# Kernel optimization log

Measured on AMD Instinct MI355X. Metric: run time of the kernel, lower is better.

## Reference

```python
import jax, jax.numpy as jnp
import numpy as np

EMBED_DIM = 1024
HEAD_DIM = 64


def setup_inputs() -> dict:
    key = jax.random.key(0)
    ks = jax.random.split(key, 7)
    s_in = EMBED_DIM ** -0.5  # torch Linear default init scale
    x = jax.random.normal(ks[0], (4, 4096, EMBED_DIM), dtype=jnp.float32)
    Wk = jax.random.uniform(ks[1], (HEAD_DIM, EMBED_DIM), jnp.float32, -s_in, s_in)
    bk = jax.random.uniform(ks[2], (HEAD_DIM,), jnp.float32, -s_in, s_in)
    Wq = jax.random.uniform(ks[3], (HEAD_DIM, EMBED_DIM), jnp.float32, -s_in, s_in)
    bq = jax.random.uniform(ks[4], (HEAD_DIM,), jnp.float32, -s_in, s_in)
    Wv = jax.random.uniform(ks[5], (HEAD_DIM, EMBED_DIM), jnp.float32, -s_in, s_in)
    bv = jax.random.uniform(ks[6], (HEAD_DIM,), jnp.float32, -s_in, s_in)
    return {"x": x, "Wq": Wq, "bq": bq, "Wk": Wk, "bk": bk, "Wv": Wv, "bv": bv}


def reference(x, Wq, bq, Wk, bk, Wv, bv):
    # torch Linear: y = x @ W.T + b
    q = jnp.einsum('btc,dc->btd', x, Wq) + bq  # [B,T,D]
    k = jnp.einsum('btc,dc->btd', x, Wk) + bk
    v = jnp.einsum('btc,dc->btd', x, Wv) + bv
    scale = HEAD_DIM ** -0.5
    # NOTE: original divides by scale (multiplies by sqrt(head_dim)) -- faithful
    scores = jnp.einsum('btd,bsd->bts', q, k) / scale  # [B,T,T]
    attn_weights = jax.nn.softmax(scores, axis=-1)
    return jnp.einsum('bts,bsd->btd', attn_weights, v)
```

## Files before the change

### kernel.cpp

```cpp
#include <hip/hip_runtime.h>

#define BATCH 4
#define SEQ   4096
#define CDIM  1024
#define DDIM  64
#define NROW  (BATCH * SEQ)
#define NSPL  8
#define SEG   (NROW * DDIM)

typedef _Float16 f16;
typedef _Float16 f16x8 __attribute__((ext_vector_type(8)));
typedef _Float16 f16x4 __attribute__((ext_vector_type(4)));
typedef __fp16   h16x2 __attribute__((ext_vector_type(2)));
typedef float    f32x4 __attribute__((ext_vector_type(4)));

#define MFMA32(a, b, c) __builtin_amdgcn_mfma_f32_16x16x32_f16((a), (b), (c), 0, 0, 0)
#define MFMA16(a, b, c) __builtin_amdgcn_mfma_f32_16x16x16f16((a), (b), (c), 0, 0, 0)

#define GLDS(g, l)                                                            \
  __builtin_amdgcn_global_load_lds((const __attribute__((address_space(1))) void*)(g), \
                                   (__attribute__((address_space(3))) void*)(l), 16, 0, 0)

#define QSCALE 11.5415603f

__device__ inline f16x8 cvt8(f32x4 a, f32x4 b) {
  h16x2 p0 = __builtin_amdgcn_cvt_pkrtz(a[0], a[1]);
  h16x2 p1 = __builtin_amdgcn_cvt_pkrtz(a[2], a[3]);
  h16x2 p2 = __builtin_amdgcn_cvt_pkrtz(b[0], b[1]);
  h16x2 p3 = __builtin_amdgcn_cvt_pkrtz(b[2], b[3]);
  f16x8 r;
  r[0] = p0[0]; r[1] = p0[1]; r[2] = p1[0]; r[3] = p1[1];
  r[4] = p2[0]; r[5] = p2[1]; r[6] = p3[0]; r[7] = p3[1];
  return r;
}

__device__ inline f16x4 cvt4(float a, float b, float c, float d) {
  h16x2 lo = __builtin_amdgcn_cvt_pkrtz(a, b);
  h16x2 hi = __builtin_amdgcn_cvt_pkrtz(c, d);
  f16x4 r;
  r[0] = lo[0]; r[1] = lo[1]; r[2] = hi[0]; r[3] = hi[1];
  return r;
}

__global__ __launch_bounds__(256) void prep_w_kernel(const float* __restrict__ Wq,
                                                     const float* __restrict__ Wk,
                                                     const float* __restrict__ Wv,
                                                     f16* __restrict__ wf2) {
  const int t = blockIdx.x * 256 + threadIdx.x;
  const int lane = t & 63;
  const int s = t >> 6;
  const int mt = s >> 5, ck = s & 31;
  const int mat = mt >> 2, tile = mt & 3;
  const int n = lane & 15, quad = lane >> 4;
  const float* W = (mat == 0) ? Wq : (mat == 1) ? Wk : Wv;
  const float* src = W + (size_t)(tile * 16 + n) * CDIM + ck * 32 + quad * 8;
  const f32x4 a = *(const f32x4*)src;
  const f32x4 b = *(const f32x4*)(src + 4);
  *(f16x8*)(wf2 + (size_t)t * 8) = cvt8(a, b);
}

__global__ __launch_bounds__(256, 4) void proj_kernel(const float* __restrict__ x,
                                                      const f16* __restrict__ wf2,
                                                      const float* __restrict__ bq,
                                                      const float* __restrict__ bk,
                                                      const float* __restrict__ bv,
                                                      f16* __restrict__ qs,
                                                      f16* __restrict__ ks,
                                                      f16* __restrict__ vc) {
  __shared__ __attribute__((aligned(16))) char lx[2][8192];
  const int tid = threadIdx.x, lane = tid & 63, w = tid >> 6;
  const int n = lane & 15, quad = lane >> 4;
  const int rowbase = blockIdx.x * 16;
  const int mtb = 3 * w;

  const float* xsrc[2];
#pragma unroll
  for (int j = 0; j < 2; ++j) {
    const int id = 2 * w + j;
    const int r = id * 2 + (lane >> 5);
    const int c = (lane & 31) ^ r;
    xsrc[j] = x + (size_t)(rowbase + r) * CDIM + c * 4;
  }

  auto issue = [&](int ck, int b) {
    char* base = &lx[b][0];
#pragma unroll
    for (int j = 0; j < 2; ++j)
      GLDS(xsrc[j] + ck * 128, base + (2 * w + j) * 1024);
  };

  const f16* wl = wf2 + (size_t)mtb * 16384 + lane * 8;

  f32x4 acc[3];
#pragma unroll
  for (int i = 0; i < 3; ++i) acc[i] = (f32x4){0.f, 0.f, 0.f, 0.f};

  issue(0, 0);
  for (int ck = 0; ck < 8; ++ck) {
    const int b = ck & 1;
    __syncthreads();
    if (ck + 1 < 8) issue(ck + 1, b ^ 1);
    const char* xb = &lx[b][0] + n * 512;
#pragma unroll
    for (int kk = 0; kk < 4; ++kk) {
      const int c1 = kk * 8 + quad * 2;
      const f32x4 xa = *(const f32x4*)(xb + ((c1 ^ n) << 4));
      const f32x4 xc = *(const f32x4*)(xb + (((c1 + 1) ^ n) << 4));
      const f16x8 af = cvt8(xa, xc);
      const f16* wq = wl + (size_t)(ck * 4 + kk) * 512;
      const f16x8 w0 = *(const f16x8*)(wq);
      const f16x8 w1 = *(const f16x8*)(wq + 16384);
      const f16x8 w2 = *(const f16x8*)(wq + 32768);
      acc[0] = MFMA32(af, w0, acc[0]);
      acc[1] = MFMA32(af, w1, acc[1]);
      acc[2] = MFMA32(af, w2, acc[2]);
    }
  }

  const int r0 = rowbase + quad * 4;
#pragma unroll
  for (int i2 = 0; i2 < 3; ++i2) {
    const int mt = mtb + i2;
    const int mat = mt >> 2, tile = mt & 3;
    const int d = tile * 16 + n;
    const f32x4 aa = acc[i2];
    if (mat == 0) {
      const float bi = bq[d];
#pragma unroll
      for (int r = 0; r < 4; ++r)
        qs[(size_t)(r0 + r) * DDIM + d] = (f16)((aa[r] + bi) * QSCALE);
    } else if (mat == 1) {
      const float bi = bk[d];
#pragma unroll
      for (int r = 0; r < 4; ++r) {
        const int tt = r0 + r;
        const int col = ((((d >> 3) ^ (tt & 7)) << 3) | (d & 7));
        ks[(size_t)tt * DDIM + col] = (f16)(aa[r] + bi);
      }
    } else {
      const float bi = bv[d];
      const int bb = r0 >> 12;
      const int tl = r0 & (SEQ - 1);
      const int ck2 = tl >> 6;
      const int bsw = (((tl & 63) >> 2) ^ n) << 2;
      *(f16x4*)(vc + ((size_t)(bb * 64 + ck2) * 64 + d) * 64 + bsw) =
          cvt4(aa[0] + bi, aa[1] + bi, aa[2] + bi, aa[3] + bi);
    }
  }
}

template <int NSPLIT>
__global__ __launch_bounds__(256, 4) void attn_kernel(const f16* __restrict__ qs,
                                                      const f16* __restrict__ ks,
                                                      const f16* __restrict__ vc,
                                                      float* __restrict__ outp,
                                                      f16* __restrict__ pacc,
                                                      float* __restrict__ pm,
                                                      float* __restrict__ pl) {
  __shared__ __attribute__((aligned(16))) f16 lk[2][4096];
  __shared__ __attribute__((aligned(16))) f16 lv[2][4096];
  const int tid = threadIdx.x, lane = tid & 63, w = tid >> 6;
  const int n = lane & 15, quad = lane >> 4;
  const int split = blockIdx.x % NSPLIT;
  const int rowblk = blockIdx.x / NSPLIT;
  const int row0 = rowblk * 128 + w * 32;
  const int bb = row0 >> 12;
  const int kbase = split * (SEQ / NSPLIT);
  const int kc0 = kbase >> 6;
  const int NC = SEQ / NSPLIT / 64;

  const f16* ksb = ks + (size_t)bb * SEQ * DDIM;
  const f16* vcb = vc + (size_t)bb * 64 * 4096;

  auto issue = [&](int c, int buf) {
#pragma unroll
    for (int i = 0; i < 2; ++i) {
      const int id = 2 * w + i;
      GLDS(ksb + (size_t)(kbase + c * 64) * 64 + id * 512 + lane * 8, &lk[buf][id * 512]);
      GLDS(vcb + (size_t)(kc0 + c) * 4096 + id * 512 + lane * 8, &lv[buf][id * 512]);
    }
  };

  f16x8 qf[2][2];
#pragma unroll
  for (int g = 0; g < 2; ++g)
#pragma unroll
    for (int hh = 0; hh < 2; ++hh)
      qf[g][hh] = *(const f16x8*)(qs + (size_t)(row0 + g * 16 + n) * DDIM + hh * 32 + quad * 8);

  const int kswz = (quad ^ (n & 7)) << 3;
  int vswz[4];
#pragma unroll
  for (int st = 0; st < 4; ++st) vswz[st] = ((((st << 2) | quad) ^ n) << 2);

  f32x4 acc[2][4];
  float m[2] = {-1e30f, -1e30f}, ll[2] = {0.f, 0.f};
#pragma unroll
  for (int g = 0; g < 2; ++g)
#pragma unroll
    for (int t = 0; t < 4; ++t) acc[g][t] = (f32x4){0.f, 0.f, 0.f, 0.f};

  issue(0, 0);
  for (int c = 0; c < NC; ++c) {
    const int b = c & 1;
    __syncthreads();
    if (c + 1 < NC) issue(c + 1, b ^ 1);

    f32x4 s[2][4];
#pragma unroll
    for (int st = 0; st < 4; ++st) {
      const f16* lkr = &lk[b][(st * 16 + n) * 64];
      const f16x8 klo = *(const f16x8*)(lkr + kswz);
      const f16x8 khi = *(const f16x8*)(lkr + (kswz ^ 32));
#pragma unroll
      for (int g = 0; g < 2; ++g) {
        f32x4 z = (f32x4){0.f, 0.f, 0.f, 0.f};
        z = MFMA32(klo, qf[g][0], z);
        s[g][st] = MFMA32(khi, qf[g][1], z);
      }
    }

    f16x4 pq[2][4];
#pragma unroll
    for (int g = 0; g < 2; ++g) {
      f32x4 mx;
#pragma unroll
      for (int r = 0; r < 4; ++r)
        mx[r] = fmaxf(fmaxf(s[g][0][r], s[g][1][r]), fmaxf(s[g][2][r], s[g][3][r]));
      float mloc = fmaxf(fmaxf(mx[0], mx[1]), fmaxf(mx[2], mx[3]));
      mloc = fmaxf(mloc, __shfl_xor(mloc, 16));
      mloc = fmaxf(mloc, __shfl_xor(mloc, 32));
      const float mnew = fmaxf(m[g], mloc);
      const float alpha = __builtin_amdgcn_exp2f(m[g] - mnew);
      m[g] = mnew;
      float psum = 0.f;
#pragma unroll
      for (int st = 0; st < 4; ++st) {
        f32x4 p;
#pragma unroll
        for (int r = 0; r < 4; ++r) p[r] = __builtin_amdgcn_exp2f(s[g][st][r] - mnew);
        psum += (p[0] + p[1]) + (p[2] + p[3]);
        pq[g][st] = cvt4(p[0], p[1], p[2], p[3]);
      }
      ll[g] = ll[g] * alpha + psum;
#pragma unroll
      for (int t = 0; t < 4; ++t) acc[g][t] *= alpha;
    }

#pragma unroll
    for (int dt = 0; dt < 4; ++dt) {
      const f16* lvr = &lv[b][(dt * 16 + n) * 64];
#pragma unroll
      for (int st = 0; st < 4; ++st) {
        const f16x4 va = *(const f16x4*)(lvr + vswz[st]);
        acc[0][dt] = MFMA16(va, pq[0][st], acc[0][dt]);
        acc[1][dt] = MFMA16(va, pq[1][st], acc[1][dt]);
      }
    }
  }

  float lred[2];
#pragma unroll
  for (int g = 0; g < 2; ++g) {
    float l = ll[g];
    l += __shfl_xor(l, 16);
    l += __shfl_xor(l, 32);
    lred[g] = l;
  }

  if (NSPLIT == 1) {
#pragma unroll
    for (int g = 0; g < 2; ++g) {
      const float inv = 1.0f / lred[g];
      const int q = row0 + g * 16 + n;
#pragma unroll
      for (int t = 0; t < 4; ++t) {
        f32x4 o = acc[g][t];
#pragma unroll
        for (int r = 0; r < 4; ++r) o[r] *= inv;
        *(f32x4*)(outp + (size_t)q * DDIM + t * 16 + quad * 4) = o;
      }
    }
  } else {
#pragma unroll
    for (int g = 0; g < 2; ++g) {
      const int q = row0 + g * 16 + n;
#pragma unroll
      for (int t = 0; t < 4; ++t)
        *(f16x4*)(pacc + ((size_t)split * NROW + q) * DDIM + t * 16 + quad * 4) =
            cvt4(acc[g][t][0], acc[g][t][1], acc[g][t][2], acc[g][t][3]);
      if (quad == 0) {
        pm[split * NROW + q] = m[g];
        pl[split * NROW + q] = lred[g];
      }
    }
  }
}

template <int NSPLIT>
__global__ __launch_bounds__(256) void combine_kernel(const f16* __restrict__ pacc,
                                                      const float* __restrict__ pm,
                                                      const float* __restrict__ pl,
                                                      float* __restrict__ out) {
  const int idx = blockIdx.x * 256 + threadIdx.x;
  const int row = idx >> 4;
  const int c = (idx & 15) * 4;
  float mm = pm[row];
#pragma unroll
  for (int s = 1; s < NSPLIT; ++s) mm = fmaxf(mm, pm[s * NROW + row]);
  float L = 0.f;
  f32x4 o = (f32x4){0.f, 0.f, 0.f, 0.f};
#pragma unroll
  for (int s = 0; s < NSPLIT; ++s) {
    const float e = __builtin_amdgcn_exp2f(pm[s * NROW + row] - mm);
    L += pl[s * NROW + row] * e;
    const f16x4 a = *(const f16x4*)(pacc + ((size_t)s * NROW + row) * DDIM + c);
#pragma unroll
    for (int j = 0; j < 4; ++j) o[j] += (float)a[j] * e;
  }
  const float inv = 1.0f / L;
#pragma unroll
  for (int j = 0; j < 4; ++j) o[j] *= inv;
  *(f32x4*)(out + (size_t)row * DDIM + c) = o;
}

extern "C" void kernel_launch(void* const* d_in, const int* in_sizes, int n_in,
                              void* d_out, int out_size, void* d_ws, size_t ws_size,
                              hipStream_t stream) {
  const float* x  = (const float*)d_in[0];
  const float* Wq = (const float*)d_in[1];
  const float* bq = (const float*)d_in[2];
  const float* Wk = (const float*)d_in[3];
  const float* bk = (const float*)d_in[4];
  const float* Wv = (const float*)d_in[5];
  const float* bv = (const float*)d_in[6];
  float* out = (float*)d_out;

  f16* wf2 = (f16*)d_ws;
  f16* qs = wf2 + 3 * 65536;
  f16* ks = qs + (size_t)SEG;
  f16* vc = ks + (size_t)SEG;
  f16* pacc = vc + (size_t)SEG;
  float* pm = (float*)(pacc + (size_t)NSPL * SEG);
  float* pl = pm + (size_t)NSPL * NROW;
  const size_t need = (size_t)((char*)(pl + (size_t)NSPL * NROW) - (char*)d_ws);

  prep_w_kernel<<<dim3(96), dim3(256), 0, stream>>>(Wq, Wk, Wv, wf2);
  proj_kernel<<<dim3(NROW / 16), dim3(256), 0, stream>>>(x, wf2, bq, bk, bv, qs, ks, vc);

  if (ws_size >= need) {
    attn_kernel<NSPL><<<dim3(128 * NSPL), dim3(256), 0, stream>>>(qs, ks, vc, nullptr, pacc, pm, pl);
    combine_kernel<NSPL><<<dim3(NROW * 16 / 256), dim3(256), 0, stream>>>(pacc, pm, pl, out);
  } else {
    attn_kernel<1><<<dim3(128), dim3(256), 0, stream>>>(qs, ks, vc, out, nullptr, nullptr, nullptr);
  }
}
```

Measured before the change: 154.5 us.

## Triple-buffer LDS prefetch with explicit vmcnt waits in projection and attention

Both the projection and attention kernels move from double to triple buffering of the LDS tiles. Loads now run two chunks ahead, and the code waits with explicit s_waitcnt vmcnt counts plus raw s_barrier instead of __syncthreads. The aim is to hide more global-to-LDS latency behind MFMA work. In exchange, the attention kernel uses more shared memory (48KB), so its launch bound drops to 3 blocks per CU, and the hand-written vmcnt counts depend on the exact number of load instructions issued.

```diff
diff --git a/kernel.cpp b/kernel.cpp
--- a/kernel.cpp
+++ b/kernel.cpp
@@ -67,7 +67,7 @@
                                                       f16* __restrict__ qs,
                                                       f16* __restrict__ ks,
                                                       f16* __restrict__ vc) {
-  __shared__ __attribute__((aligned(16))) char lx[2][8192];
+  __shared__ __attribute__((aligned(16))) char lx[3 * 8192];
   const int tid = threadIdx.x, lane = tid & 63, w = tid >> 6;
   const int n = lane & 15, quad = lane >> 4;
   const int rowbase = blockIdx.x * 16;
@@ -82,8 +82,8 @@
     xsrc[j] = x + (size_t)(rowbase + r) * CDIM + c * 4;
   }
 
-  auto issue = [&](int ck, int b) {
-    char* base = &lx[b][0];
+  auto issue = [&](int ck, int bufi) {
+    char* base = &lx[bufi * 8192];
 #pragma unroll
     for (int j = 0; j < 2; ++j)
       GLDS(xsrc[j] + ck * 128, base + (2 * w + j) * 1024);
@@ -96,11 +96,16 @@
   for (int i = 0; i < 3; ++i) acc[i] = (f32x4){0.f, 0.f, 0.f, 0.f};
 
   issue(0, 0);
+  issue(1, 1);
   for (int ck = 0; ck < 8; ++ck) {
-    const int b = ck & 1;
-    __syncthreads();
-    if (ck + 1 < 8) issue(ck + 1, b ^ 1);
-    const char* xb = &lx[b][0] + n * 512;
+    const int bufi = ck % 3;
+    if (ck + 2 < 8) issue(ck + 2, (ck + 2) % 3);
+    if (ck + 2 < 8)      asm volatile("s_waitcnt vmcnt(4)" ::: "memory");
+    else if (ck + 1 < 8) asm volatile("s_waitcnt vmcnt(2)" ::: "memory");
+    else                 asm volatile("s_waitcnt vmcnt(0)" ::: "memory");
+    __builtin_amdgcn_s_barrier();
+    __builtin_amdgcn_sched_barrier(0);
+    const char* xb = &lx[bufi * 8192] + n * 512;
 #pragma unroll
     for (int kk = 0; kk < 4; ++kk) {
       const int c1 = kk * 8 + quad * 2;
@@ -115,6 +120,7 @@
       acc[1] = MFMA32(af, w1, acc[1]);
       acc[2] = MFMA32(af, w2, acc[2]);
     }
+    __builtin_amdgcn_s_barrier();
   }
 
   const int r0 = rowbase + quad * 4;
@@ -150,15 +156,15 @@
 }
 
 template <int NSPLIT>
-__global__ __launch_bounds__(256, 4) void attn_kernel(const f16* __restrict__ qs,
+__global__ __launch_bounds__(256, 3) void attn_kernel(const f16* __restrict__ qs,
                                                       const f16* __restrict__ ks,
                                                       const f16* __restrict__ vc,
                                                       float* __restrict__ outp,
                                                       f16* __restrict__ pacc,
                                                       float* __restrict__ pm,
                                                       float* __restrict__ pl) {
-  __shared__ __attribute__((aligned(16))) f16 lk[2][4096];
-  __shared__ __attribute__((aligned(16))) f16 lv[2][4096];
+  __shared__ __attribute__((aligned(16))) f16 lk[3 * 4096];
+  __shared__ __attribute__((aligned(16))) f16 lv[3 * 4096];
   const int tid = threadIdx.x, lane = tid & 63, w = tid >> 6;
   const int n = lane & 15, quad = lane >> 4;
   const int split = blockIdx.x % NSPLIT;
@@ -172,12 +178,14 @@
   const f16* ksb = ks + (size_t)bb * SEQ * DDIM;
   const f16* vcb = vc + (size_t)bb * 64 * 4096;
 
-  auto issue = [&](int c, int buf) {
+  auto issue = [&](int c, int bufi) {
 #pragma unroll
     for (int i = 0; i < 2; ++i) {
       const int id = 2 * w + i;
-      GLDS(ksb + (size_t)(kbase + c * 64) * 64 + id * 512 + lane * 8, &lk[buf][id * 512]);
-      GLDS(vcb + (size_t)(kc0 + c) * 4096 + id * 512 + lane * 8, &lv[buf][id * 512]);
+      GLDS(ksb + (size_t)(kbase + c * 64) * 64 + id * 512 + lane * 8,
+           &lk[bufi * 4096 + id * 512]);
+      GLDS(vcb + (size_t)(kc0 + c) * 4096 + id * 512 + lane * 8,
+           &lv[bufi * 4096 + id * 512]);
     }
   };
 
@@ -201,15 +209,20 @@
     for (int t = 0; t < 4; ++t) acc[g][t] = (f32x4){0.f, 0.f, 0.f, 0.f};
 
   issue(0, 0);
+  issue(1, 1);
   for (int c = 0; c < NC; ++c) {
-    const int b = c & 1;
-    __syncthreads();
-    if (c + 1 < NC) issue(c + 1, b ^ 1);
+    const int bufi = c % 3;
+    if (c + 2 < NC) issue(c + 2, (c + 2) % 3);
+    if (c + 2 < NC)      asm volatile("s_waitcnt vmcnt(8)" ::: "memory");
+    else if (c + 1 < NC) asm volatile("s_waitcnt vmcnt(4)" ::: "memory");
+    else                 asm volatile("s_waitcnt vmcnt(0)" ::: "memory");
+    __builtin_amdgcn_s_barrier();
+    __builtin_amdgcn_sched_barrier(0);
 
     f32x4 s[2][4];
 #pragma unroll
     for (int st = 0; st < 4; ++st) {
-      const f16* lkr = &lk[b][(st * 16 + n) * 64];
+      const f16* lkr = &lk[bufi * 4096 + (st * 16 + n) * 64];
       const f16x8 klo = *(const f16x8*)(lkr + kswz);
       const f16x8 khi = *(const f16x8*)(lkr + (kswz ^ 32));
 #pragma unroll
@@ -249,7 +262,7 @@
 
 #pragma unroll
     for (int dt = 0; dt < 4; ++dt) {
-      const f16* lvr = &lv[b][(dt * 16 + n) * 64];
+      const f16* lvr = &lv[bufi * 4096 + (dt * 16 + n) * 64];
 #pragma unroll
       for (int st = 0; st < 4; ++st) {
         const f16x4 va = *(const f16x4*)(lvr + vswz[st]);
@@ -257,6 +270,7 @@
         acc[1][dt] = MFMA16(va, pq[1][st], acc[1][dt]);
       }
     }
+    __builtin_amdgcn_s_barrier();
   }
 
   float lred[2];
```

New measurement: 155.1 us. Within noise of the previous version (+0.4%).
